# Kernel tuning notes

Measured on AMD Instinct MI355X. Metric: run time of the kernel, lower is better.

The kernel has to match this reference:

```python
import jax, jax.numpy as jnp
import numpy as np

C = 256
NUM_HEADS = 4
NBLK = 6  # 3 stages x depth 2
WS = (2, 8, 8)   # 3D window
SS = (1, 4, 4)   # shift for odd blocks
N_WIN = WS[0] * WS[1] * WS[2]  # 128 tokens per window
RPB_SIZE = (2 * WS[0] - 1) * (2 * WS[1] - 1) * (2 * WS[2] - 1)  # 675


def _rel_index():
    coords = np.stack(np.meshgrid(np.arange(WS[0]), np.arange(WS[1]), np.arange(WS[2]), indexing='ij'))
    coords = coords.reshape(3, -1)
    rel = (coords[:, :, None] - coords[:, None, :]).transpose(1, 2, 0)
    rel[:, :, 0] += WS[0] - 1
    rel[:, :, 1] += WS[1] - 1
    rel[:, :, 2] += WS[2] - 1
    rel[:, :, 0] *= (2 * WS[1] - 1) * (2 * WS[2] - 1)
    rel[:, :, 1] *= (2 * WS[2] - 1)
    return jnp.asarray(rel.sum(-1))  # [N_WIN, N_WIN]

REL_IDX = _rel_index()


def window_partition(x):
    # [B,D,H,W,C] -> [B*nW, N_WIN, C]
    B, D, H, W, Cc = x.shape
    x = x.reshape(B, D // WS[0], WS[0], H // WS[1], WS[1], W // WS[2], WS[2], Cc)
    return x.transpose(0, 1, 3, 5, 2, 4, 6, 7).reshape(-1, N_WIN, Cc)


def window_reverse(win, B, D, H, W):
    Cc = win.shape[-1]
    x = win.reshape(B, D // WS[0], H // WS[1], W // WS[2], WS[0], WS[1], WS[2], Cc)
    return x.transpose(0, 1, 4, 2, 5, 3, 6, 7).reshape(B, D, H, W, Cc)


def attn_mask(D, H, W):
    # standard shifted-window mask, computed on host constants
    img = np.zeros((1, D, H, W, 1), np.float32)
    cnt = 0
    for d in (slice(0, -WS[0]), slice(-WS[0], -SS[0]), slice(-SS[0], None)):
        for h in (slice(0, -WS[1]), slice(-WS[1], -SS[1]), slice(-SS[1], None)):
            for w in (slice(0, -WS[2]), slice(-WS[2], -SS[2]), slice(-SS[2], None)):
                img[:, d, h, w, :] = cnt
                cnt += 1
    mw = img.reshape(1, D // WS[0], WS[0], H // WS[1], WS[1], W // WS[2], WS[2], 1)
    mw = mw.transpose(0, 1, 3, 5, 2, 4, 6, 7).reshape(-1, N_WIN)
    diff = mw[:, None, :] - mw[:, :, None]
    return jnp.asarray(np.where(diff != 0, -100.0, 0.0).astype(np.float32))  # [nW,N,N]


def layer_norm(x, g, b):
    mu = x.mean(-1, keepdims=True)
    var = ((x - mu) ** 2).mean(-1, keepdims=True)
    return (x - mu) * jax.lax.rsqrt(var + 1e-5) * g + b


def setup_inputs() -> dict:
    key = jax.random.key(0)
    ks = jax.random.split(key, 10)
    f = jax.random.normal
    s = 0.02
    return dict(
        x=f(ks[0], (2, 2, 2, 4096, C), jnp.float32),
        n1w=jnp.ones((NBLK, C), jnp.float32), n1b=jnp.zeros((NBLK, C), jnp.float32),
        qkv_w=f(ks[1], (NBLK, C, 3 * C), jnp.float32) * s, qkv_b=jnp.zeros((NBLK, 3 * C), jnp.float32),
        rpb=f(ks[2], (NBLK, RPB_SIZE, NUM_HEADS), jnp.float32) * s,
        proj_w=f(ks[3], (NBLK, C, C), jnp.float32) * s, proj_b=jnp.zeros((NBLK, C), jnp.float32),
        n2w=jnp.ones((NBLK, C), jnp.float32), n2b=jnp.zeros((NBLK, C), jnp.float32),
        mlp1_w=f(ks[4], (NBLK, C, 4 * C), jnp.float32) * s, mlp1_b=jnp.zeros((NBLK, 4 * C), jnp.float32),
        mlp2_w=f(ks[5], (NBLK, 4 * C, C), jnp.float32) * s, mlp2_b=jnp.zeros((NBLK, C), jnp.float32),
        exp_v_w=f(ks[6], (C, 2 * C), jnp.float32) * s,
        exp_v_nw=jnp.ones((C,), jnp.float32), exp_v_nb=jnp.zeros((C,), jnp.float32),
        exp_t_w=f(ks[7], (C, 2 * C), jnp.float32) * s,
        exp_t_nw=jnp.ones((C,), jnp.float32), exp_t_nb=jnp.zeros((C,), jnp.float32),
    )


def reference(x, n1w, n1b, qkv_w, qkv_b, rpb, proj_w, proj_b, n2w, n2b,
              mlp1_w, mlp1_b, mlp2_w, mlp2_b,
              exp_v_w, exp_v_nw, exp_v_nb, exp_t_w, exp_t_nw, exp_t_nb):
    B, T, V, L, _ = x.shape
    H = W = int(round(np.sqrt(L)))
    NH = NUM_HEADS
    dh = C // NH

    def block(h, i, D, shifted, mask):
        # h: [B, D, L, C]
        sc = h
        y = layer_norm(h, n1w[i], n1b[i]).reshape(B, D, H, W, C)
        if shifted:
            y = jnp.roll(y, (-SS[0], -SS[1], -SS[2]), axis=(1, 2, 3))
        win = window_partition(y)  # [B*nW, N, C]
        qkv = (win @ qkv_w[i] + qkv_b[i]).reshape(-1, N_WIN, 3, NH, dh)
        q, k, v = jnp.moveaxis(qkv, 2, 0)              # [B*nW, N, NH, dh]
        q = q.transpose(0, 2, 1, 3)
        k = k.transpose(0, 2, 1, 3)
        v = v.transpose(0, 2, 1, 3)                     # [B*nW, NH, N, dh]
        attn = jnp.einsum('whqd,whkd->whqk', q, k) * (dh ** -0.5)
        attn = attn + rpb[i][REL_IDX].transpose(2, 0, 1)[None]
        if mask is not None:
            nW = mask.shape[0]
            attn = attn.reshape(B, nW, NH, N_WIN, N_WIN) + mask[None, :, None]
            attn = attn.reshape(-1, NH, N_WIN, N_WIN)
        attn = jax.nn.softmax(attn, axis=-1)
        out = jnp.einsum('whqk,whkd->whqd', attn, v).transpose(0, 2, 1, 3).reshape(-1, N_WIN, C)
        out = out @ proj_w[i] + proj_b[i]
        y = window_reverse(out, B, D, H, W)
        if shifted:
            y = jnp.roll(y, (SS[0], SS[1], SS[2]), axis=(1, 2, 3))
        h = sc + y.reshape(B, D, L, C)
        z = layer_norm(h, n2w[i], n2b[i])
        z = jax.nn.gelu(z @ mlp1_w[i] + mlp1_b[i], approximate=False) @ mlp2_w[i] + mlp2_b[i]
        return h + z

    def stage(h, i0, D):
        mask = attn_mask(D, H, W)
        h = block(h, i0, D, False, None)
        h = block(h, i0 + 1, D, True, mask)
        return h

    # stage 1: swin over D = T*V
    h = x.reshape(B, T * V, L, C)
    h = stage(h, 0, T * V)
    h = h.reshape(B, T, V, L, C)

    # stage 2: view patch expand (V -> 2V) + swin
    h = (h @ exp_v_w).reshape(B, T, V, L, 2, C).transpose(0, 1, 2, 4, 3, 5).reshape(B, T, 2 * V, L, C)
    h = layer_norm(h, exp_v_nw, exp_v_nb)
    V2 = 2 * V
    h = h.reshape(B, T * V2, L, C)
    h = stage(h, 2, T * V2)
    h = h.reshape(B, T, V2, L, C)

    # stage 3: temporal patch expand (T -> 2T) + swin
    h = (h @ exp_t_w).reshape(B, T, V2, L, 2, C).transpose(0, 1, 4, 2, 3, 5).reshape(B, 2 * T, V2, L, C)
    h = layer_norm(h, exp_t_nw, exp_t_nb)
    T2 = 2 * T
    h = h.reshape(B, T2 * V2, L, C)
    h = stage(h, 4, T2 * V2)
    return h.reshape(B, T2, V2, L, C)
```

## Files before the change

### kernel.cpp

```cpp
#include <hip/hip_runtime.h>

typedef __bf16 bf16x8 __attribute__((ext_vector_type(8)));
typedef float f32x4 __attribute__((ext_vector_type(4)));
typedef unsigned short u16;
typedef unsigned int u32;

__device__ __forceinline__ u16 f2b(float f) {
    union { float f; u32 u; } v; v.f = f;
    u32 r = v.u + 0x7fffu + ((v.u >> 16) & 1u);
    return (u16)(r >> 16);
}
__device__ __forceinline__ float b2f(u16 u) {
    union { u32 u; float f; } v; v.u = ((u32)u) << 16; return v.f;
}
__device__ __forceinline__ void gl_lds16(const u16* g, u16* l) {
    __builtin_amdgcn_global_load_lds(
        (const __attribute__((address_space(1))) void*)g,
        (__attribute__((address_space(3))) void*)l, 16, 0, 0);
}

__global__ __launch_bounds__(256) void ln_kernel(
    const float* __restrict__ h, u16* __restrict__ out,
    const float* __restrict__ g, const float* __restrict__ bb,
    int D, int dsh, int shifted, int mode)
{
    const int lane = threadIdx.x & 63;
    const int t = blockIdx.x * 4 + (threadIdx.x >> 6);
    const float4 xv = *(const float4*)(h + (size_t)t * 256 + lane * 4);
    float s = xv.x + xv.y + xv.z + xv.w;
    float s2 = xv.x*xv.x + xv.y*xv.y + xv.z*xv.z + xv.w*xv.w;
    #pragma unroll
    for (int o = 32; o > 0; o >>= 1) { s += __shfl_xor(s, o); s2 += __shfl_xor(s2, o); }
    const float mu = s * 0.00390625f;
    const float var = s2 * 0.00390625f - mu * mu;
    const float rs = 1.0f / sqrtf(var + 1e-5f);
    const int c0 = lane * 4;
    const float4 gv = *(const float4*)(g + c0);
    const float4 bv = *(const float4*)(bb + c0);
    ushort4 o4;
    o4.x = f2b((xv.x - mu) * rs * gv.x + bv.x);
    o4.y = f2b((xv.y - mu) * rs * gv.y + bv.y);
    o4.z = f2b((xv.z - mu) * rs * gv.z + bv.z);
    o4.w = f2b((xv.w - mu) * rs * gv.w + bv.w);
    size_t oidx;
    if (mode == 1) {
        oidx = (size_t)t * 256 + c0;
    } else {
        const int b = t >> (dsh + 12);
        const int rem = t & ((1 << (dsh + 12)) - 1);
        int d = rem >> 12;
        const int l = rem & 4095;
        int hh = l >> 6, ww = l & 63;
        if (shifted) { d = d ? d - 1 : D - 1; hh = (hh - 4) & 63; ww = (ww - 4) & 63; }
        const int widx = (b << (dsh + 5)) + ((d >> 1) << 6) + ((hh >> 3) << 3) + (ww >> 3);
        const int n = ((d & 1) << 6) + ((hh & 7) << 3) + (ww & 7);
        oidx = ((size_t)(widx * 128 + n)) * 256 + c0;
    }
    *(ushort4*)(out + oidx) = o4;
}

__global__ __launch_bounds__(256) void cast_kernel(const float* __restrict__ in, u16* __restrict__ out, int n4)
{
    const int i = blockIdx.x * 256 + threadIdx.x;
    if (i >= n4) return;
    const float4 v = ((const float4*)in)[i];
    ushort4 o; o.x = f2b(v.x); o.y = f2b(v.y); o.z = f2b(v.z); o.w = f2b(v.w);
    ((ushort4*)out)[i] = o;
}

__global__ __launch_bounds__(256) void wt_kernel(const float* __restrict__ src, u16* __restrict__ dst, int K, int N)
{
    const size_t base = (size_t)blockIdx.y * K * N;
    const int idx = blockIdx.x * 256 + threadIdx.x;
    const int k = idx / N, n = idx - k * N;
    dst[base + (size_t)n * K + k] = f2b(src[base + idx]);
}

struct GemmP {
    const u16* A; const u16* Bt;
    int K;
    const float* bias;
    u16* outb;
    float* outf;
    const float* hin; float* hout;
    int D, shifted, nwsh, row_off;
};

template <int EPI>
__global__ __launch_bounds__(256, 2) void gemm_kernel(GemmP p)
{
    __shared__ __align__(16) char smem[33792];
    float* CF = (float*)smem;

    const int tid = threadIdx.x;
    const int m0 = blockIdx.x * 128, n0 = blockIdx.y * 128;
    const int K = p.K;
    const int lane = tid & 63;
    const int wv = tid >> 6;
    const int wm = (wv & 1) * 64, wn = (wv >> 1) * 64;
    const int l16 = lane & 15, quad = lane >> 4;

    f32x4 acc[4][4];
    #pragma unroll
    for (int a = 0; a < 4; a++)
        #pragma unroll
        for (int b = 0; b < 4; b++)
            acc[a][b] = f32x4{0.f, 0.f, 0.f, 0.f};

    const int lrow = lane >> 2;
    const int c16s = (lane & 3) ^ (lrow & 3);
    const int rA0 = wv * 16;
    const u16* Ag = p.A + (size_t)(m0 + rA0 + lrow) * K + c16s * 8;
    const u16* Bg = p.Bt + (size_t)(n0 + rA0 + lrow) * K + c16s * 8;
    const size_t j64 = (size_t)64 * K;
    const int fslot = (quad ^ (l16 & 3)) * 8;

    {
        u16* Al = (u16*)smem + rA0 * 32;
        u16* Bl = (u16*)(smem + 8192) + rA0 * 32;
        gl_lds16(Ag, Al);
        gl_lds16(Ag + j64, Al + 64 * 32);
        gl_lds16(Bg, Bl);
        gl_lds16(Bg + j64, Bl + 64 * 32);
    }
    __syncthreads();

    int kb = 0;
    for (int k0 = 0; k0 < K; k0 += 32, kb ^= 1) {
        if (k0 + 32 < K) {
            char* nb = smem + (kb ^ 1) * 16384;
            u16* Al = (u16*)nb + rA0 * 32;
            u16* Bl = (u16*)(nb + 8192) + rA0 * 32;
            gl_lds16(Ag + k0 + 32, Al);
            gl_lds16(Ag + j64 + k0 + 32, Al + 64 * 32);
            gl_lds16(Bg + k0 + 32, Bl);
            gl_lds16(Bg + j64 + k0 + 32, Bl + 64 * 32);
        }
        const u16* As = (const u16*)(smem + kb * 16384);
        const u16* Bs = (const u16*)(smem + kb * 16384 + 8192);
        bf16x8 af[4], bfr[4];
        #pragma unroll
        for (int mt = 0; mt < 4; mt++) af[mt] = *(const bf16x8*)(As + (wm + mt * 16 + l16) * 32 + fslot);
        #pragma unroll
        for (int nt = 0; nt < 4; nt++) bfr[nt] = *(const bf16x8*)(Bs + (wn + nt * 16 + l16) * 32 + fslot);
        #pragma unroll
        for (int mt = 0; mt < 4; mt++)
            #pragma unroll
            for (int nt = 0; nt < 4; nt++)
                acc[mt][nt] = __builtin_amdgcn_mfma_f32_16x16x32_bf16(af[mt], bfr[nt], acc[mt][nt], 0, 0, 0);
        __syncthreads();
    }

    const int crow = tid >> 2;
    const int p4 = (tid & 3) * 4;
    #pragma unroll
    for (int c = 0; c < 2; c++) {
        if (c) __syncthreads();
        if ((wv & 1) == c) {
            #pragma unroll
            for (int mt = 0; mt < 4; mt++)
                #pragma unroll
                for (int nt = 0; nt < 4; nt++)
                    #pragma unroll
                    for (int i = 0; i < 4; i++)
                        CF[(mt * 16 + quad * 4 + i) * 132 + wn + nt * 16 + l16] = acc[mt][nt][i];
        }
        __syncthreads();
        const int rowg = m0 + c * 64 + crow;
        size_t tokbase = 0;
        if constexpr (EPI == 1) {
            const int widx = rowg >> 7, n = rowg & 127;
            const int b = widx >> p.nwsh, rem = widx & ((1 << p.nwsh) - 1);
            int dd = ((rem >> 6) << 1) + (n >> 6);
            int hh = (((rem >> 3) & 7) << 3) + ((n >> 3) & 7);
            int ww = ((rem & 7) << 3) + (n & 7);
            if (p.shifted) { dd = (dd + 1 == p.D) ? 0 : dd + 1; hh = (hh + 4) & 63; ww = (ww + 4) & 63; }
            tokbase = ((size_t)((b * p.D + dd) * 4096 + hh * 64 + ww)) * 256;
        } else if constexpr (EPI == 3) {
            tokbase = (size_t)(p.row_off + rowg) * 256;
        }
        #pragma unroll
        for (int j = 0; j < 8; j++) {
            const int colf = j * 16 + p4;
            const int colg = n0 + colf;
            const float4 t = *(const float4*)(CF + crow * 132 + colf);
            const float4 bi = (EPI <= 3) ? *(const float4*)(p.bias + colg) : float4{0.f,0.f,0.f,0.f};
            if constexpr (EPI == 0) {
                const float sc = (colg < 256) ? 0.125f : 1.0f;
                ushort4 pk;
                pk.x = f2b((t.x + bi.x) * sc);
                pk.y = f2b((t.y + bi.y) * sc);
                pk.z = f2b((t.z + bi.z) * sc);
                pk.w = f2b((t.w + bi.w) * sc);
                *(ushort4*)(p.outb + (size_t)rowg * 768 + colg) = pk;
            } else if constexpr (EPI == 1 || EPI == 3) {
                const float* hi = p.hin + tokbase + colg;
                float* ho = p.hout + tokbase + colg;
                const float4 r = *(const float4*)hi;
                float4 o;
                o.x = r.x + t.x + bi.x;
                o.y = r.y + t.y + bi.y;
                o.z = r.z + t.z + bi.z;
                o.w = r.w + t.w + bi.w;
                *(float4*)ho = o;
            } else if constexpr (EPI == 2) {
                float4 g4;
                g4.x = t.x + bi.x; g4.y = t.y + bi.y; g4.z = t.z + bi.z; g4.w = t.w + bi.w;
                ushort4 pk;
                pk.x = f2b(0.5f * g4.x * (1.0f + erff(g4.x * 0.7071067811865475f)));
                pk.y = f2b(0.5f * g4.y * (1.0f + erff(g4.y * 0.7071067811865475f)));
                pk.z = f2b(0.5f * g4.z * (1.0f + erff(g4.z * 0.7071067811865475f)));
                pk.w = f2b(0.5f * g4.w * (1.0f + erff(g4.w * 0.7071067811865475f)));
                *(ushort4*)(p.outb + (size_t)rowg * 1024 + colg) = pk;
            } else {
                *(float4*)(p.outf + (size_t)rowg * 512 + colg) = t;
            }
        }
    }
}

__global__ __launch_bounds__(256, 2) void attn_mfma_kernel(
    const u16* __restrict__ qkv, u16* __restrict__ att,
    const float* __restrict__ rpbp, int D, int shifted, int w0g, int nwsh)
{
    __shared__ __align__(16) char smem[57856];
    u16* Qs = (u16*)smem;
    u16* Ks = (u16*)(smem + 18432);
    u16* Ps = (u16*)smem;
    u16* Vt = (u16*)(smem + 36864);
    float* rb = (float*)(smem + 54272);
    int* lbl = (int*)(smem + 56972);

    const int wloc = blockIdx.x;
    const int head = blockIdx.y;
    const int tid = threadIdx.x;
    const u16* base = qkv + (size_t)wloc * 98304;

    #pragma unroll
    for (int it = 0; it < 4; it++) {
        const int id = it * 256 + tid;
        const int row = id >> 3, oct = id & 7;
        const size_t ro = (size_t)row * 768 + head * 64 + oct * 8;
        *(uint4*)(Qs + row * 72 + oct * 8) = *(const uint4*)(base + ro);
        *(uint4*)(Ks + row * 72 + oct * 8) = *(const uint4*)(base + ro + 256);
        uint4 vv = *(const uint4*)(base + ro + 512);
        const u16* vp = (const u16*)&vv;
        #pragma unroll
        for (int q = 0; q < 8; q++) Vt[(oct * 8 + q) * 136 + row] = vp[q];
    }
    for (int j = tid; j < 675; j += 256) rb[j] = rpbp[j * 4 + head];
    if (tid < 128) {
        int lv = 0;
        if (shifted) {
            const int widx = w0g + wloc;
            const int rem = widx & ((1 << nwsh) - 1);
            const int d0 = rem >> 6, h0 = (rem >> 3) & 7, w0 = rem & 7;
            const int wd = tid >> 6, wh = (tid >> 3) & 7, ww = tid & 7;
            const int rd = (d0 < (D >> 1) - 1) ? 0 : (1 + wd);
            const int rh = (h0 < 7) ? 0 : (1 + (wh >= 4));
            const int rw = (w0 < 7) ? 0 : (1 + (ww >= 4));
            lv = rd * 9 + rh * 3 + rw;
        }
        lbl[tid] = lv;
    }
    __syncthreads();

    const int wq = tid >> 6;
    const int lane = tid & 63;
    const int l16 = lane & 15, quad = lane >> 4;
    const int myrow0 = wq * 32;

    f32x4 sc[2][8];
    #pragma unroll
    for (int mt = 0; mt < 2; mt++)
        #pragma unroll
        for (int nt = 0; nt < 8; nt++)
            sc[mt][nt] = f32x4{0.f, 0.f, 0.f, 0.f};
    #pragma unroll
    for (int kt = 0; kt < 2; kt++) {
        bf16x8 aq[2];
        #pragma unroll
        for (int mt = 0; mt < 2; mt++)
            aq[mt] = *(const bf16x8*)(Qs + (myrow0 + mt * 16 + l16) * 72 + kt * 32 + quad * 8);
        bf16x8 bk[8];
        #pragma unroll
        for (int nt = 0; nt < 8; nt++)
            bk[nt] = *(const bf16x8*)(Ks + (nt * 16 + l16) * 72 + kt * 32 + quad * 8);
        #pragma unroll
        for (int mt = 0; mt < 2; mt++)
            #pragma unroll
            for (int nt = 0; nt < 8; nt++)
                sc[mt][nt] = __builtin_amdgcn_mfma_f32_16x16x32_bf16(aq[mt], bk[nt], sc[mt][nt], 0, 0, 0);
    }

    float linv[2][4];
    #pragma unroll
    for (int mt = 0; mt < 2; mt++) {
        #pragma unroll
        for (int i = 0; i < 4; i++) {
            const int row = myrow0 + mt * 16 + quad * 4 + i;
            const int rbase = ((row >> 6) + 1) * 225 + (((row >> 3) & 7) + 7) * 15 + ((row & 7) + 7);
            const int lq = lbl[row];
            float mx = -1e30f;
            float sv[8];
            #pragma unroll
            for (int nt = 0; nt < 8; nt++) {
                const int col = nt * 16 + l16;
                float v = sc[mt][nt][i] + rb[rbase - (col >> 6) * 225 - ((col >> 3) & 7) * 15 - (col & 7)];
                if (shifted && lq != lbl[col]) v -= 100.0f;
                sv[nt] = v;
                mx = fmaxf(mx, v);
            }
            #pragma unroll
            for (int o = 1; o < 16; o <<= 1) mx = fmaxf(mx, __shfl_xor(mx, o));
            float l = 0.0f;
            #pragma unroll
            for (int nt = 0; nt < 8; nt++) {
                const float pp = __expf(sv[nt] - mx);
                sc[mt][nt][i] = pp;
                l += pp;
            }
            #pragma unroll
            for (int o = 1; o < 16; o <<= 1) l += __shfl_xor(l, o);
            linv[mt][i] = 1.0f / l;
        }
    }

    __syncthreads();
    #pragma unroll
    for (int mt = 0; mt < 2; mt++)
        #pragma unroll
        for (int nt = 0; nt < 8; nt++)
            #pragma unroll
            for (int i = 0; i < 4; i++)
                Ps[(myrow0 + mt * 16 + quad * 4 + i) * 136 + nt * 16 + l16] = f2b(sc[mt][nt][i]);

    f32x4 oc[2][4];
    #pragma unroll
    for (int mt = 0; mt < 2; mt++)
        #pragma unroll
        for (int nt = 0; nt < 4; nt++)
            oc[mt][nt] = f32x4{0.f, 0.f, 0.f, 0.f};
    #pragma unroll
    for (int kt = 0; kt < 4; kt++) {
        bf16x8 ap[2];
        #pragma unroll
        for (int mt = 0; mt < 2; mt++)
            ap[mt] = *(const bf16x8*)(Ps + (myrow0 + mt * 16 + l16) * 136 + kt * 32 + quad * 8);
        bf16x8 bv[4];
        #pragma unroll
        for (int nt = 0; nt < 4; nt++)
            bv[nt] = *(const bf16x8*)(Vt + (nt * 16 + l16) * 136 + kt * 32 + quad * 8);
        #pragma unroll
        for (int mt = 0; mt < 2; mt++)
            #pragma unroll
            for (int nt = 0; nt < 4; nt++)
                oc[mt][nt] = __builtin_amdgcn_mfma_f32_16x16x32_bf16(ap[mt], bv[nt], oc[mt][nt], 0, 0, 0);
    }

    #pragma unroll
    for (int mt = 0; mt < 2; mt++)
        #pragma unroll
        for (int nt = 0; nt < 4; nt++)
            #pragma unroll
            for (int i = 0; i < 4; i++) {
                const int row = myrow0 + mt * 16 + quad * 4 + i;
                const int col = nt * 16 + l16;
                att[(size_t)(wloc * 128 + row) * 256 + head * 64 + col] = f2b(oc[mt][nt][i] * linv[mt][i]);
            }
}

__global__ __launch_bounds__(256) void expand_ln_kernel(
    const float* __restrict__ sc, float* __restrict__ hout,
    const float* __restrict__ g, const float* __restrict__ bb,
    int it0, int typ)
{
    const int lane = threadIdx.x & 63;
    const int ot = blockIdx.x * 4 + (threadIdx.x >> 6);
    const int itl = ot >> 1, e = ot & 1;
    const float4 xv = *(const float4*)(sc + (size_t)itl * 512 + e * 256 + lane * 4);
    float s = xv.x + xv.y + xv.z + xv.w;
    float s2 = xv.x*xv.x + xv.y*xv.y + xv.z*xv.z + xv.w*xv.w;
    #pragma unroll
    for (int o = 32; o > 0; o >>= 1) { s += __shfl_xor(s, o); s2 += __shfl_xor(s2, o); }
    const float mu = s * 0.00390625f;
    const float var = s2 * 0.00390625f - mu * mu;
    const float rs = 1.0f / sqrtf(var + 1e-5f);
    const int c0 = lane * 4;
    const float4 gv = *(const float4*)(g + c0);
    const float4 bv = *(const float4*)(bb + c0);
    float4 y;
    y.x = (xv.x - mu) * rs * gv.x + bv.x;
    y.y = (xv.y - mu) * rs * gv.y + bv.y;
    y.z = (xv.z - mu) * rs * gv.z + bv.z;
    y.w = (xv.w - mu) * rs * gv.w + bv.w;
    const int it = it0 + itl;
    size_t otg;
    if (typ == 0) {
        const int b = it >> 14, rr = it & 16383;
        const int t = rr >> 13, v = (rr >> 12) & 1, l = rr & 4095;
        otg = (size_t)(((b * 2 + t) * 4 + v * 2 + e) * 4096 + l);
    } else {
        const int b = it >> 15, rr = it & 32767;
        const int t = rr >> 14, v2 = (rr >> 12) & 3, l = rr & 4095;
        otg = (size_t)(((b * 4 + t * 2 + e) * 4 + v2) * 4096 + l);
    }
    *(float4*)(hout + otg * 256 + c0) = y;
}

extern "C" void kernel_launch(void* const* d_in, const int* in_sizes, int n_in,
                              void* d_out, int out_size, void* d_ws, size_t ws_size,
                              hipStream_t stream)
{
    const float* x      = (const float*)d_in[0];
    const float* n1w    = (const float*)d_in[1];
    const float* n1b    = (const float*)d_in[2];
    const float* qkv_w  = (const float*)d_in[3];
    const float* qkv_b  = (const float*)d_in[4];
    const float* rpb    = (const float*)d_in[5];
    const float* proj_w = (const float*)d_in[6];
    const float* proj_b = (const float*)d_in[7];
    const float* n2w    = (const float*)d_in[8];
    const float* n2b    = (const float*)d_in[9];
    const float* mlp1_w = (const float*)d_in[10];
    const float* mlp1_b = (const float*)d_in[11];
    const float* mlp2_w = (const float*)d_in[12];
    const float* mlp2_b = (const float*)d_in[13];
    const float* expv_w = (const float*)d_in[14];
    const float* expv_nw= (const float*)d_in[15];
    const float* expv_nb= (const float*)d_in[16];
    const float* expt_w = (const float*)d_in[17];
    const float* expt_nw= (const float*)d_in[18];
    const float* expt_nb= (const float*)d_in[19];
    (void)in_sizes; (void)n_in; (void)out_size;

    if (ws_size < 352321536ULL) return;

    char* ws = (char*)d_ws;
    float* h    = (float*)ws;
    u16*  winb  = (u16*)(ws + 134217728LL);
    u16*  att   = (u16*)(ws + 134217728LL + 67108864LL);
    char* scr   = ws + 134217728LL + 2LL * 67108864LL;
    u16*  scrb  = (u16*)scr;
    float* scrf = (float*)scr;
    u16* qkvT   = (u16*)(ws + 134217728LL + 3LL * 67108864LL);
    u16* projT  = qkvT + 6 * 768 * 256;
    u16* mlp1T  = projT + 6 * 256 * 256;
    u16* mlp2T  = mlp1T + 6 * 1024 * 256;
    u16* expvT  = mlp2T + 6 * 256 * 1024;
    u16* exptT  = expvT + 512 * 256;

    wt_kernel<<<dim3(768, 6), 256, 0, stream>>>(qkv_w, qkvT, 256, 768);
    wt_kernel<<<dim3(256, 6), 256, 0, stream>>>(proj_w, projT, 256, 256);
    wt_kernel<<<dim3(1024, 6), 256, 0, stream>>>(mlp1_w, mlp1T, 256, 1024);
    wt_kernel<<<dim3(1024, 6), 256, 0, stream>>>(mlp2_w, mlp2T, 1024, 256);
    wt_kernel<<<dim3(512, 1), 256, 0, stream>>>(expv_w, expvT, 256, 512);
    wt_kernel<<<dim3(512, 1), 256, 0, stream>>>(expt_w, exptT, 256, 512);
    hipMemcpyAsync(h, x, 33554432ULL, hipMemcpyDeviceToDevice, stream);

    for (int s = 0; s < 3; s++) {
        const int D = 4 << s;
        const int dsh = 2 + s;
        const int nwsh = dsh + 5;
        const int tokens = 2 * D * 4096;
        const int nch = tokens / 32768;
        for (int j = 0; j < 2; j++) {
            const int i = 2 * s + j;
            ln_kernel<<<dim3(tokens / 4), 256, 0, stream>>>(h, winb, n1w + i * 256, n1b + i * 256, D, dsh, j, 0);
            for (int c = 0; c < nch; c++) {
                GemmP gq{};
                gq.A = winb + (size_t)c * 32768 * 256;
                gq.Bt = qkvT + (size_t)i * 768 * 256;
                gq.K = 256; gq.bias = qkv_b + i * 768; gq.outb = scrb;
                gemm_kernel<0><<<dim3(256, 6), 256, 0, stream>>>(gq);
                attn_mfma_kernel<<<dim3(256, 4), 256, 0, stream>>>(scrb, att + (size_t)c * 32768 * 256,
                                                                   rpb + i * 675 * 4, D, j, c * 256, nwsh);
            }
            GemmP gp{};
            gp.A = att; gp.Bt = projT + (size_t)i * 256 * 256; gp.K = 256;
            gp.bias = proj_b + i * 256; gp.hin = h; gp.hout = h;
            gp.D = D; gp.shifted = j; gp.nwsh = nwsh;
            gemm_kernel<1><<<dim3(tokens / 128, 2), 256, 0, stream>>>(gp);
            ln_kernel<<<dim3(tokens / 4), 256, 0, stream>>>(h, winb, n2w + i * 256, n2b + i * 256, D, dsh, 0, 1);
            for (int c = 0; c < nch; c++) {
                GemmP g1{};
                g1.A = winb + (size_t)c * 32768 * 256;
                g1.Bt = mlp1T + (size_t)i * 1024 * 256;
                g1.K = 256; g1.bias = mlp1_b + i * 1024; g1.outb = scrb;
                gemm_kernel<2><<<dim3(256, 8), 256, 0, stream>>>(g1);
                GemmP g2{};
                g2.A = scrb; g2.Bt = mlp2T + (size_t)i * 256 * 1024; g2.K = 1024;
                g2.bias = mlp2_b + i * 256; g2.hin = h; g2.row_off = c * 32768;
                g2.hout = (s == 2 && j == 1) ? (float*)d_out : h;
                gemm_kernel<3><<<dim3(256, 2), 256, 0, stream>>>(g2);
            }
        }
        if (s < 2) {
            const int ntok = tokens;
            cast_kernel<<<dim3(ntok * 64 / 256), 256, 0, stream>>>(h, winb, ntok * 64);
            const u16* eT = (s == 0) ? expvT : exptT;
            const float* eg = (s == 0) ? expv_nw : expt_nw;
            const float* eb = (s == 0) ? expv_nb : expt_nb;
            for (int c = 0; c < ntok / 32768; c++) {
                GemmP ge{};
                ge.A = winb + (size_t)c * 32768 * 256; ge.Bt = eT; ge.K = 256; ge.outf = scrf;
                gemm_kernel<4><<<dim3(256, 4), 256, 0, stream>>>(ge);
                expand_ln_kernel<<<dim3(16384), 256, 0, stream>>>(scrf, h, eg, eb, c * 32768, s);
            }
        }
    }
}
```

Before: 2.808 ms.

## Fuse MLP fc1, GELU and fc2 into one kernel keeping hidden in LDS

```diff
diff --git a/kernel.cpp b/kernel.cpp
--- a/kernel.cpp
+++ b/kernel.cpp
@@ -219,6 +219,141 @@
     }
 }
 
+struct MlpP {
+    const u16* A;
+    const u16* W1t;
+    const u16* W2t;
+    const float* b1;
+    const float* b2;
+    const float* hin;
+    float* hout;
+};
+
+__global__ __launch_bounds__(512, 2) void mlp_fused_kernel(MlpP p)
+{
+    __shared__ __align__(16) char smem[135168];
+    u16* As = (u16*)smem;
+    float* CF = (float*)(smem + 65536);
+
+    const int tid = threadIdx.x;
+    const int lane = tid & 63;
+    const int wv = tid >> 6;
+    const int l16 = lane & 15, quad = lane >> 4;
+    const int tok0 = blockIdx.x * 128;
+
+    const int wm = (wv & 3) * 32;
+    const int wn1 = (wv >> 2) * 64;
+    const int wn2 = (wv >> 2) * 128;
+    const int fslot = (quad ^ (l16 & 3)) * 8;
+
+    {
+        const int lrow = lane >> 2;
+        const int cs = (lane & 3) ^ (lrow & 3);
+        const u16* Ag = p.A + (size_t)(tok0 + wv * 16 + lrow) * 256 + cs * 8;
+        u16* Al = As + wv * 512;
+        #pragma unroll
+        for (int pk = 0; pk < 8; pk++)
+            gl_lds16(Ag + pk * 32, Al + pk * 4096);
+    }
+
+    f32x4 acc2[2][8];
+    #pragma unroll
+    for (int mt = 0; mt < 2; mt++)
+        #pragma unroll
+        for (int nt = 0; nt < 8; nt++)
+            acc2[mt][nt] = f32x4{0.f, 0.f, 0.f, 0.f};
+
+    float b2v[8];
+    #pragma unroll
+    for (int nt = 0; nt < 8; nt++) b2v[nt] = p.b2[wn2 + nt * 16 + l16];
+
+    __syncthreads();
+
+    for (int c = 0; c < 8; c++) {
+        f32x4 acc1[2][4];
+        #pragma unroll
+        for (int mt = 0; mt < 2; mt++)
+            #pragma unroll
+            for (int nt = 0; nt < 4; nt++)
+                acc1[mt][nt] = f32x4{0.f, 0.f, 0.f, 0.f};
+        const u16* w1b = p.W1t + (size_t)(c * 128 + wn1 + l16) * 256 + quad * 8;
+        #pragma unroll
+        for (int kt = 0; kt < 8; kt++) {
+            bf16x8 af[2], bfr[4];
+            #pragma unroll
+            for (int mt = 0; mt < 2; mt++)
+                af[mt] = *(const bf16x8*)(As + kt * 4096 + (wm + mt * 16 + l16) * 32 + fslot);
+            #pragma unroll
+            for (int nt = 0; nt < 4; nt++)
+                bfr[nt] = *(const bf16x8*)(w1b + (size_t)nt * 4096 + kt * 32);
+            #pragma unroll
+            for (int mt = 0; mt < 2; mt++)
+                #pragma unroll
+                for (int nt = 0; nt < 4; nt++)
+                    acc1[mt][nt] = __builtin_amdgcn_mfma_f32_16x16x32_bf16(af[mt], bfr[nt], acc1[mt][nt], 0, 0, 0);
+        }
+
+        u16* Sb = (u16*)(smem + 65536 + (c & 1) * 34816);
+        #pragma unroll
+        for (int nt = 0; nt < 4; nt++) {
+            const float b1v = p.b1[c * 128 + wn1 + nt * 16 + l16];
+            #pragma unroll
+            for (int mt = 0; mt < 2; mt++)
+                #pragma unroll
+                for (int i = 0; i < 4; i++) {
+                    const float x = acc1[mt][nt][i] + b1v;
+                    const float g = 0.5f * x * (1.0f + erff(x * 0.7071067811865475f));
+                    Sb[(wm + mt * 16 + quad * 4 + i) * 136 + wn1 + nt * 16 + l16] = f2b(g);
+                }
+        }
+        __syncthreads();
+
+        const u16* w2b = p.W2t + (size_t)(wn2 + l16) * 1024 + c * 128 + quad * 8;
+        #pragma unroll
+        for (int kt = 0; kt < 4; kt++) {
+            bf16x8 ap[2], bv[8];
+            #pragma unroll
+            for (int mt = 0; mt < 2; mt++)
+                ap[mt] = *(const bf16x8*)(Sb + (wm + mt * 16 + l16) * 136 + kt * 32 + quad * 8);
+            #pragma unroll
+            for (int nt = 0; nt < 8; nt++)
+                bv[nt] = *(const bf16x8*)(w2b + (size_t)nt * 16384 + kt * 32);
+            #pragma unroll
+            for (int mt = 0; mt < 2; mt++)
+                #pragma unroll
+                for (int nt = 0; nt < 8; nt++)
+                    acc2[mt][nt] = __builtin_amdgcn_mfma_f32_16x16x32_bf16(ap[mt], bv[nt], acc2[mt][nt], 0, 0, 0);
+        }
+    }
+
+    #pragma unroll
+    for (int cc = 0; cc < 2; cc++) {
+        __syncthreads();
+        if (((wv & 3) >> 1) == cc) {
+            const int rb = wm & 63;
+            #pragma unroll
+            for (int mt = 0; mt < 2; mt++)
+                #pragma unroll
+                for (int nt = 0; nt < 8; nt++)
+                    #pragma unroll
+                    for (int i = 0; i < 4; i++)
+                        CF[(rb + mt * 16 + quad * 4 + i) * 260 + wn2 + nt * 16 + l16] = acc2[mt][nt][i] + b2v[nt];
+        }
+        __syncthreads();
+        #pragma unroll
+        for (int jj = 0; jj < 8; jj++) {
+            const int idx = jj * 512 + tid;
+            const int row = idx >> 6, c4 = (idx & 63) << 2;
+            const size_t g = (size_t)(tok0 + cc * 64 + row) * 256 + c4;
+            const float4 t = *(const float4*)(CF + row * 260 + c4);
+            const float4 r = *(const float4*)(p.hin + g);
+            float4 o;
+            o.x = t.x + r.x; o.y = t.y + r.y; o.z = t.z + r.z; o.w = t.w + r.w;
+            *(float4*)(p.hout + g) = o;
+        }
+    }
+}
+
 __global__ __launch_bounds__(256, 2) void attn_mfma_kernel(
     const u16* __restrict__ qkv, u16* __restrict__ att,
     const float* __restrict__ rpbp, int D, int shifted, int w0g, int nwsh)
@@ -482,18 +617,15 @@
             gp.D = D; gp.shifted = j; gp.nwsh = nwsh;
             gemm_kernel<1><<<dim3(tokens / 128, 2), 256, 0, stream>>>(gp);
             ln_kernel<<<dim3(tokens / 4), 256, 0, stream>>>(h, winb, n2w + i * 256, n2b + i * 256, D, dsh, 0, 1);
-            for (int c = 0; c < nch; c++) {
-                GemmP g1{};
-                g1.A = winb + (size_t)c * 32768 * 256;
-                g1.Bt = mlp1T + (size_t)i * 1024 * 256;
-                g1.K = 256; g1.bias = mlp1_b + i * 1024; g1.outb = scrb;
-                gemm_kernel<2><<<dim3(256, 8), 256, 0, stream>>>(g1);
-                GemmP g2{};
-                g2.A = scrb; g2.Bt = mlp2T + (size_t)i * 256 * 1024; g2.K = 1024;
-                g2.bias = mlp2_b + i * 256; g2.hin = h; g2.row_off = c * 32768;
-                g2.hout = (s == 2 && j == 1) ? (float*)d_out : h;
-                gemm_kernel<3><<<dim3(256, 2), 256, 0, stream>>>(g2);
-            }
+            MlpP mp{};
+            mp.A = winb;
+            mp.W1t = mlp1T + (size_t)i * 1024 * 256;
+            mp.W2t = mlp2T + (size_t)i * 256 * 1024;
+            mp.b1 = mlp1_b + i * 1024;
+            mp.b2 = mlp2_b + i * 256;
+            mp.hin = h;
+            mp.hout = (s == 2 && j == 1) ? (float*)d_out : h;
+            mlp_fused_kernel<<<dim3(tokens / 128), 512, 0, stream>>>(mp);
         }
         if (s < 2) {
             const int ntok = tokens;
```

Result: slower. 3.715 ms (+32.3%).
